# Optimization experiments

Measured on AMD Instinct MI355X. Metric: run time of the kernel, lower is better.

Reference implementation:

```python
import jax, jax.numpy as jnp
import numpy as np

EPS = 1e-5


def setup_inputs() -> dict:
    key = jax.random.key(0)
    ks = jax.random.split(key, 6)
    B, N, F = 8, 8192, 64
    xyzs = jax.random.uniform(ks[0], (B, N, 3), dtype=jnp.float32)
    feats = jax.random.normal(ks[1], (B, N, F), dtype=jnp.float32)
    c_in = 3 + F  # 67
    dims = [(64, c_in), (64, 64), (128, 64)]
    inp = {"xyzs": xyzs, "feats": feats}
    for i, (co, ci) in enumerate(dims, start=1):
        inp[f"w{i}"] = jax.random.normal(ks[1 + i], (co, ci), dtype=jnp.float32) / np.sqrt(ci)
        inp[f"b{i}"] = jnp.zeros((co,), jnp.float32)
        inp[f"g{i}"] = jnp.ones((co,), jnp.float32)
        inp[f"bt{i}"] = jnp.zeros((co,), jnp.float32)
        inp[f"m{i}"] = jnp.zeros((co,), jnp.float32)
        inp[f"v{i}"] = jnp.ones((co,), jnp.float32)
    return inp


def sample_farthest_points(xyz, S):
    # Iterative FPS starting from index 0 (pytorch3d default random_start_point=False).
    B, N, _ = xyz.shape
    barange = jnp.arange(B)

    def step(carry, _):
        mind, last = carry                      # mind: [B,N] min sq-dist to selected set
        lastp = xyz[barange, last]              # [B,3]
        d = jnp.sum((xyz - lastp[:, None, :]) ** 2, -1)
        mind = jnp.minimum(mind, d)
        nxt = jnp.argmax(mind, axis=1).astype(jnp.int32)
        return (mind, nxt), nxt

    init = (jnp.full((B, N), 1e10, xyz.dtype), jnp.zeros((B,), jnp.int32))
    _, rest = jax.lax.scan(step, init, None, length=S - 1)  # [S-1, B]
    idx = jnp.concatenate([jnp.zeros((1, B), jnp.int32), rest], 0).T  # [B,S]
    return xyz[barange[:, None], idx], idx


def ball_query(centers, xyz, K, radius):
    # First-K-in-radius semantics of pytorch3d.ops.ball_query; pad idx with -1,
    # pad gathered points with zeros (masked_gather behavior).
    B, N, _ = xyz.shape
    d2 = (jnp.sum(centers ** 2, -1)[:, :, None]
          + jnp.sum(xyz ** 2, -1)[:, None, :]
          - 2.0 * jnp.einsum('bsd,bnd->bsn', centers, xyz))  # [B,S,N]
    within = d2 <= radius * radius
    skey = jnp.where(within, jnp.arange(N, dtype=jnp.int32), N)
    negvals, idx = jax.lax.top_k(-skey, K)      # K smallest keys = first K in-radius
    valid = (-negvals) < N                       # [B,S,K]
    group_idx = jnp.where(valid, idx, -1)
    gathered = xyz[jnp.arange(B)[:, None, None], jnp.where(valid, idx, 0)]  # [B,S,K,3]
    group_xyz = jnp.where(valid[..., None], gathered, 0.0)
    return group_idx, group_xyz


def _mlp_layer(x, w, b, g, bt, m, v):
    # 1x1 Conv2d over channel axis + BatchNorm (eval stats) + ReLU; x: [B,S,K,Cin]
    y = jnp.einsum('bskc,oc->bsko', x, w) + b
    y = g * (y - m) * jax.lax.rsqrt(v + EPS) + bt
    return jax.nn.relu(y)


def reference(xyzs, feats, w1, b1, g1, bt1, m1, v1,
              w2, b2, g2, bt2, m2, v2, w3, b3, g3, bt3, m3, v3):
    S, K, radius = 2048, 32, 0.2
    B = xyzs.shape[0]
    center_xyzs, _ = sample_farthest_points(xyzs, S)             # [B,S,3]
    group_idxs, group_xyzs = ball_query(center_xyzs, xyzs, K, radius)
    group_xyzs = group_xyzs - center_xyzs[:, :, None, :]          # relative coords
    batch_idxs = jnp.arange(B)[:, None, None]
    gf = feats[batch_idxs, jnp.where(group_idxs < 0, 0, group_idxs)]  # [B,S,K,F]
    gf = jnp.concatenate([group_xyzs, gf], axis=-1)
    gf = gf * (group_idxs != -1)[..., None].astype(gf.dtype)      # zero padded slots
    x = _mlp_layer(gf, w1, b1, g1, bt1, m1, v1)
    x = _mlp_layer(x, w2, b2, g2, bt2, m2, v2)
    x = _mlp_layer(x, w3, b3, g3, bt3, m3, v3)
    center_feats = jnp.max(x, axis=2)                             # max over neighbors
    return center_xyzs, center_feats
```

## Files before the change

### kernel.cpp

```cpp
#include <hip/hip_runtime.h>


#define NPTS 8192
#define SCTR 2048
#define NB   8
#define KNN  32
#define NF   64

typedef float v2f __attribute__((ext_vector_type(2)));

__device__ __forceinline__ v2f pk_add(v2f a, v2f b) {
  v2f r; asm("v_pk_add_f32 %0, %1, %2" : "=v"(r) : "v"(a), "v"(b)); return r;
}
__device__ __forceinline__ v2f pk_mul(v2f a, v2f b) {
  v2f r; asm("v_pk_mul_f32 %0, %1, %2" : "=v"(r) : "v"(a), "v"(b)); return r;
}

__device__ __forceinline__ float sumsq3(float x, float y, float z) {
#pragma clang fp contract(off)
  return (x * x + y * y) + z * z;
}

__device__ __forceinline__ float bq_d2(float sc, float sx,
                                       float cx, float cy, float cz,
                                       float x, float y, float z) {
#pragma clang fp contract(off)
  float dt = fmaf(cz, z, fmaf(cy, y, cx * x));
  return (sc + sx) - 2.0f * dt;
}

template <int CTRL>
__device__ __forceinline__ unsigned long long kmax_dpp(unsigned long long k) {
  int lo = (int)(unsigned int)(k & 0xFFFFFFFFull);
  int hi = (int)(unsigned int)(k >> 32);
  int slo = __builtin_amdgcn_update_dpp(lo, lo, CTRL, 0xF, 0xF, false);
  int shi = __builtin_amdgcn_update_dpp(hi, hi, CTRL, 0xF, 0xF, false);
  unsigned long long sk =
      ((unsigned long long)(unsigned int)shi << 32) | (unsigned int)slo;
  return sk > k ? sk : k;
}

__global__ __launch_bounds__(256, 1) void fps_transpose_kernel(
    const float* __restrict__ xyzs,
    const float* __restrict__ w1, const float* __restrict__ w2, const float* __restrict__ w3,
    float* __restrict__ centers, float* __restrict__ wT)
{
  const int t = threadIdx.x;
  if (blockIdx.x >= NB) {
    int idx = (blockIdx.x - NB) * 256 + t;
    if (idx < 67*64) {
      int c = idx >> 6, o = idx & 63;
      wT[idx] = w1[o*67 + c];
    } else if (idx < 67*64 + 64*64) {
      int r = idx - 67*64; int c = r >> 6, o = r & 63;
      wT[idx] = w2[o*64 + c];
    } else if (idx < 67*64 + 64*64 + 64*128) {
      int r = idx - (67*64 + 64*64); int c = r >> 7, o = r & 127;
      wT[idx] = w3[o*64 + c];
    }
    return;
  }

  const int b = blockIdx.x;
  const float* xb = xyzs + (size_t)b * NPTS * 3;

  __shared__ float sX[NPTS], sY[NPTS], sZ[NPTS];
  __shared__ unsigned long long redk[2][4];
  __shared__ int hist[SCTR];

  for (int i = t; i < NPTS; i += 256) {
    sX[i] = xb[3*i+0];
    sY[i] = xb[3*i+1];
    sZ[i] = xb[3*i+2];
  }
  if (t == 0) hist[0] = 0;
  __syncthreads();

  const int t4 = 4 * t;

  const float4 xA = *(const float4*)(sX + 0    + t4);
  const float4 yA = *(const float4*)(sY + 0    + t4);
  const float4 zA = *(const float4*)(sZ + 0    + t4);
  const float4 xB = *(const float4*)(sX + 1024 + t4);
  const float4 yB = *(const float4*)(sY + 1024 + t4);
  const float4 zB = *(const float4*)(sZ + 1024 + t4);
  const float4 xC = *(const float4*)(sX + 2048 + t4);
  const float4 yC = *(const float4*)(sY + 2048 + t4);
  const float4 zC = *(const float4*)(sZ + 2048 + t4);
  const float4 xD = *(const float4*)(sX + 3072 + t4);
  const float4 yD = *(const float4*)(sY + 3072 + t4);
  const float4 zD = *(const float4*)(sZ + 3072 + t4);
  const float4 xE = *(const float4*)(sX + 4096 + t4);
  const float4 yE = *(const float4*)(sY + 4096 + t4);
  const float4 zE = *(const float4*)(sZ + 4096 + t4);
  const float4 xF = *(const float4*)(sX + 5120 + t4);
  const float4 yF = *(const float4*)(sY + 5120 + t4);
  const float4 zF = *(const float4*)(sZ + 5120 + t4);
  const float4 xG = *(const float4*)(sX + 6144 + t4);
  const float4 yG = *(const float4*)(sY + 6144 + t4);
  const float4 zG = *(const float4*)(sZ + 6144 + t4);
  const float4 xH = *(const float4*)(sX + 7168 + t4);
  const float4 yH = *(const float4*)(sY + 7168 + t4);
  const float4 zH = *(const float4*)(sZ + 7168 + t4);

  float4 mA = make_float4(1e10f,1e10f,1e10f,1e10f);
  float4 mB = mA, mC = mA, mD = mA, mE = mA, mF = mA, mG = mA, mH = mA;

  float lx = sX[0], ly = sY[0], lz = sZ[0];

#define FPS_HALF(PX0, PX1, PY0, PY1, PZ0, PZ1, MM0, MM1, I0, I1, BV, BG)     \
  do {                                                                       \
    v2f px_ = {PX0, PX1}, py_ = {PY0, PY1}, pz_ = {PZ0, PZ1};               \
    v2f dx_ = pk_add(px_, nlx);                                              \
    v2f dy_ = pk_add(py_, nly);                                              \
    v2f dz_ = pk_add(pz_, nlz);                                              \
    v2f dd_ = pk_add(pk_add(pk_mul(dx_,dx_), pk_mul(dy_,dy_)),               \
                     pk_mul(dz_,dz_));                                       \
    MM0 = fminf(MM0, dd_.x); if (MM0 > BV) { BV = MM0; BG = (I0); }          \
    MM1 = fminf(MM1, dd_.y); if (MM1 > BV) { BV = MM1; BG = (I1); }          \
  } while (0)

#define FPS_QUAD(QX, QY, QZ, MV, QOFF, BV, BG)                               \
  do {                                                                       \
    FPS_HALF(QX.x, QX.y, QY.x, QY.y, QZ.x, QZ.y, MV.x, MV.y,                 \
             (QOFF)+t4+0, (QOFF)+t4+1, BV, BG);                              \
    FPS_HALF(QX.z, QX.w, QY.z, QY.w, QZ.z, QZ.w, MV.z, MV.w,                 \
             (QOFF)+t4+2, (QOFF)+t4+3, BV, BG);                              \
  } while (0)

  for (int s = 1; s < SCTR; ++s) {
    float bv0 = -1.0f, bv1 = -1.0f; int bg0 = 0, bg1 = 0;
    {
      v2f nlx = {-lx, -lx}, nly = {-ly, -ly}, nlz = {-lz, -lz};
      FPS_QUAD(xA, yA, zA, mA, 0,    bv0, bg0);
      FPS_QUAD(xB, yB, zB, mB, 1024, bv0, bg0);
      FPS_QUAD(xC, yC, zC, mC, 2048, bv0, bg0);
      FPS_QUAD(xD, yD, zD, mD, 3072, bv0, bg0);
      FPS_QUAD(xE, yE, zE, mE, 4096, bv1, bg1);
      FPS_QUAD(xF, yF, zF, mF, 5120, bv1, bg1);
      FPS_QUAD(xG, yG, zG, mG, 6144, bv1, bg1);
      FPS_QUAD(xH, yH, zH, mH, 7168, bv1, bg1);
    }
    float bv = bv0; int bg = bg0;
    if (bv1 > bv0) { bv = bv1; bg = bg1; }

    unsigned long long key =
        ((unsigned long long)__float_as_uint(bv) << 13) |
        (unsigned long long)(8191 - bg);

    key = kmax_dpp<0x111>(key);
    key = kmax_dpp<0x112>(key);
    key = kmax_dpp<0x114>(key);
    key = kmax_dpp<0x118>(key);
    key = kmax_dpp<0x142>(key);
    key = kmax_dpp<0x143>(key);

    int pb = s & 1;
    if ((t & 63) == 63) redk[pb][t >> 6] = key;
    __syncthreads();

    unsigned long long k4 = redk[pb][t & 3];
    k4 = kmax_dpp<0xB1>(k4);
    k4 = kmax_dpp<0x4E>(k4);

    int i0 = 8191 - (int)(k4 & 0x1FFFull);
    lx = sX[i0]; ly = sY[i0]; lz = sZ[i0];
    if (t == 0) hist[s] = i0;
  }
#undef FPS_QUAD
#undef FPS_HALF
  __syncthreads();

  for (int s = t; s < SCTR; s += 256) {
    int i = hist[s];
    float* o = centers + ((size_t)b * SCTR + s) * 3;
    o[0] = sX[i]; o[1] = sY[i]; o[2] = sZ[i];
  }
}

__global__ __launch_bounds__(128) void sa_fused_kernel(
    const float* __restrict__ xyzs, const float* __restrict__ feats,
    const float* centers, const float* __restrict__ wT,
    const float* __restrict__ b1, const float* __restrict__ g1, const float* __restrict__ bt1,
    const float* __restrict__ m1, const float* __restrict__ v1,
    const float* __restrict__ b2, const float* __restrict__ g2, const float* __restrict__ bt2,
    const float* __restrict__ m2, const float* __restrict__ v2,
    const float* __restrict__ b3, const float* __restrict__ g3, const float* __restrict__ bt3,
    const float* __restrict__ m3, const float* __restrict__ v3,
    float* out_feats)
{
  constexpr float R2 = (float)(0.2 * 0.2);
  const int bid  = blockIdx.x;
  const int b    = bid >> 11;
  const int tid  = threadIdx.x;
  const int w    = tid >> 6;
  const int lane = tid & 63;
  const float* xb = xyzs + (size_t)b * NPTS * 3;
  const float* cp = centers + (size_t)bid * 3;
  float cx = cp[0], cy = cp[1], cz = cp[2];
  float sc = sumsq3(cx, cy, cz);

  __shared__ int   gidx[KNN];
  __shared__ float in_[32*67];
  __shared__ float y_[32*65];

  int cnt = 0;
  for (int base = 0; base < NPTS && cnt < KNN; base += 64) {
    int n = base + lane;
    float x = xb[n*3+0], y = xb[n*3+1], z = xb[n*3+2];
    float sx = sumsq3(x, y, z);
    float d2 = bq_d2(sc, sx, cx, cy, cz, x, y, z);
    bool within = (d2 <= R2);
    unsigned long long mk = __ballot(within);
    int rank = __popcll(mk & ((1ull << lane) - 1ull));
    int slot = cnt + rank;
    if (within && slot < KNN) gidx[slot] = n;
    cnt += (int)__popcll(mk);
  }
  if (cnt > KNN) cnt = KNN;
  __syncthreads();

#pragma unroll 4
  for (int k2 = 0; k2 < 16; ++k2) {
    int k = 2*k2 + w;
    int gk = (k < cnt) ? gidx[k] : -1;
    float fv = 0.f, xv = 0.f;
    if (gk >= 0) {
      fv = feats[((size_t)b * NPTS + gk) * NF + lane];
      if (lane < 3) xv = xb[gk*3 + lane] - cp[lane];
    }
    in_[k*67 + 3 + lane] = fv;
    if (lane < 3) in_[k*67 + lane] = xv;
  }
  __syncthreads();

  const int g = lane >> 3;
  const int h = lane & 7;
  const float* w1T = wT;
  const float* w2T = wT + 67*64;
  const float* w3T = wT + 67*64 + 64*64;

  {
    float acc[4][4];
#pragma unroll
    for (int i=0;i<4;++i)
#pragma unroll
      for (int j=0;j<4;++j) acc[i][j]=0.f;
#pragma unroll 4
    for (int c = 0; c < 67; ++c) {
      float a0 = in_[(4*g+0)*67 + c];
      float a1 = in_[(4*g+1)*67 + c];
      float a2 = in_[(4*g+2)*67 + c];
      float a3 = in_[(4*g+3)*67 + c];
      float4 wv = *(const float4*)(w1T + c*64 + w*32 + 4*h);
      float wj[4] = {wv.x, wv.y, wv.z, wv.w};
#pragma unroll
      for (int j=0;j<4;++j) {
        acc[0][j] = fmaf(a0, wj[j], acc[0][j]);
        acc[1][j] = fmaf(a1, wj[j], acc[1][j]);
        acc[2][j] = fmaf(a2, wj[j], acc[2][j]);
        acc[3][j] = fmaf(a3, wj[j], acc[3][j]);
      }
    }
    float scl[4], shf[4];
#pragma unroll
    for (int j=0;j<4;++j) {
      int o = w*32 + 4*h + j;
      float r = g1[o] * rsqrtf(v1[o] + 1e-5f);
      scl[j] = r;
      shf[j] = (b1[o] - m1[o]) * r + bt1[o];
    }
#pragma unroll
    for (int i=0;i<4;++i) {
      int k = 4*g + i;
#pragma unroll
      for (int j=0;j<4;++j)
        y_[k*65 + w*32 + 4*h + j] = fmaxf(fmaf(acc[i][j], scl[j], shf[j]), 0.f);
    }
  }
  __syncthreads();

  {
    float acc[4][4];
#pragma unroll
    for (int i=0;i<4;++i)
#pragma unroll
      for (int j=0;j<4;++j) acc[i][j]=0.f;
#pragma unroll 4
    for (int c = 0; c < 64; ++c) {
      float a0 = y_[(4*g+0)*65 + c];
      float a1 = y_[(4*g+1)*65 + c];
      float a2 = y_[(4*g+2)*65 + c];
      float a3 = y_[(4*g+3)*65 + c];
      float4 wv = *(const float4*)(w2T + c*64 + w*32 + 4*h);
      float wj[4] = {wv.x, wv.y, wv.z, wv.w};
#pragma unroll
      for (int j=0;j<4;++j) {
        acc[0][j] = fmaf(a0, wj[j], acc[0][j]);
        acc[1][j] = fmaf(a1, wj[j], acc[1][j]);
        acc[2][j] = fmaf(a2, wj[j], acc[2][j]);
        acc[3][j] = fmaf(a3, wj[j], acc[3][j]);
      }
    }
    float scl[4], shf[4];
#pragma unroll
    for (int j=0;j<4;++j) {
      int o = w*32 + 4*h + j;
      float r = g2[o] * rsqrtf(v2[o] + 1e-5f);
      scl[j] = r;
      shf[j] = (b2[o] - m2[o]) * r + bt2[o];
    }
    __syncthreads();
#pragma unroll
    for (int i=0;i<4;++i) {
      int k = 4*g + i;
#pragma unroll
      for (int j=0;j<4;++j)
        in_[k*65 + w*32 + 4*h + j] = fmaxf(fmaf(acc[i][j], scl[j], shf[j]), 0.f);
    }
  }
  __syncthreads();

  for (int p = 0; p < 2; ++p) {
    float acc[4][4];
#pragma unroll
    for (int i=0;i<4;++i)
#pragma unroll
      for (int j=0;j<4;++j) acc[i][j]=0.f;
#pragma unroll 4
    for (int c = 0; c < 64; ++c) {
      float a0 = in_[(4*g+0)*65 + c];
      float a1 = in_[(4*g+1)*65 + c];
      float a2 = in_[(4*g+2)*65 + c];
      float a3 = in_[(4*g+3)*65 + c];
      float4 wv = *(const float4*)(w3T + c*128 + w*64 + p*32 + 4*h);
      float wj[4] = {wv.x, wv.y, wv.z, wv.w};
#pragma unroll
      for (int j=0;j<4;++j) {
        acc[0][j] = fmaf(a0, wj[j], acc[0][j]);
        acc[1][j] = fmaf(a1, wj[j], acc[1][j]);
        acc[2][j] = fmaf(a2, wj[j], acc[2][j]);
        acc[3][j] = fmaf(a3, wj[j], acc[3][j]);
      }
    }
    float scl[4], shf[4];
#pragma unroll
    for (int j=0;j<4;++j) {
      int o = w*64 + p*32 + 4*h + j;
      float r = g3[o] * rsqrtf(v3[o] + 1e-5f);
      scl[j] = r;
      shf[j] = (b3[o] - m3[o]) * r + bt3[o];
    }
    float vm[4];
#pragma unroll
    for (int j=0;j<4;++j) {
      float q0 = fmaxf(fmaf(acc[0][j], scl[j], shf[j]), 0.f);
      float q1 = fmaxf(fmaf(acc[1][j], scl[j], shf[j]), 0.f);
      float q2 = fmaxf(fmaf(acc[2][j], scl[j], shf[j]), 0.f);
      float q3 = fmaxf(fmaf(acc[3][j], scl[j], shf[j]), 0.f);
      vm[j] = fmaxf(fmaxf(q0,q1), fmaxf(q2,q3));
    }
#pragma unroll
    for (int mk = 8; mk < 64; mk <<= 1) {
#pragma unroll
      for (int j=0;j<4;++j) vm[j] = fmaxf(vm[j], __shfl_xor(vm[j], mk));
    }
    if (g == 0) {
      float* dst = out_feats + (size_t)bid*128 + w*64 + p*32 + 4*h;
      *(float4*)dst = make_float4(vm[0], vm[1], vm[2], vm[3]);
    }
  }
}

extern "C" void kernel_launch(void* const* d_in, const int* in_sizes, int n_in,
                              void* d_out, int out_size, void* d_ws, size_t ws_size,
                              hipStream_t stream) {
  const float* xyzs  = (const float*)d_in[0];
  const float* feats = (const float*)d_in[1];
  const float* w1  = (const float*)d_in[2];
  const float* b1  = (const float*)d_in[3];
  const float* g1  = (const float*)d_in[4];
  const float* bt1 = (const float*)d_in[5];
  const float* m1  = (const float*)d_in[6];
  const float* v1  = (const float*)d_in[7];
  const float* w2  = (const float*)d_in[8];
  const float* b2  = (const float*)d_in[9];
  const float* g2  = (const float*)d_in[10];
  const float* bt2 = (const float*)d_in[11];
  const float* m2  = (const float*)d_in[12];
  const float* v2  = (const float*)d_in[13];
  const float* w3  = (const float*)d_in[14];
  const float* b3  = (const float*)d_in[15];
  const float* g3  = (const float*)d_in[16];
  const float* bt3 = (const float*)d_in[17];
  const float* m3  = (const float*)d_in[18];
  const float* v3  = (const float*)d_in[19];

  float* out       = (float*)d_out;
  float* centers   = out;
  float* out_feats = out + (size_t)NB * SCTR * 3;
  float* wT        = (float*)d_ws;

  hipLaunchKernelGGL(fps_transpose_kernel, dim3(NB + 65), dim3(256), 0, stream,
                     xyzs, w1, w2, w3, centers, wT);
  hipLaunchKernelGGL(sa_fused_kernel, dim3(NB * SCTR), dim3(128), 0, stream,
                     xyzs, feats, centers, wT,
                     b1, g1, bt1, m1, v1,
                     b2, g2, bt2, m2, v2,
                     b3, g3, bt3, m3, v3,
                     out_feats);
}
```

Before: 2.389 ms.

## Pad MLP activation rows to 68 for float4 LDS access; scalarize FPS distance

Shared-memory activation buffers are padded from 67/65 to 68-float rows. The MLP inner loops now read four channels at once with float4 LDS loads, take four weight rows per step, and write outputs as float4, which cuts the number of LDS instructions. The first layer zero-fills column 67 and loops to 68, so it reads one row past the end of w1T (the start of w2T); that read is harmless because it is multiplied by zero. The FPS loop also drops the inline-asm packed v_pk_add/v_pk_mul math in favour of plain scalar distance code with contraction off, which may change instruction count in the serial FPS phase.

```diff
diff --git a/kernel.cpp b/kernel.cpp
--- a/kernel.cpp
+++ b/kernel.cpp
@@ -7,18 +7,18 @@
 #define KNN  32
 #define NF   64
 
-typedef float v2f __attribute__((ext_vector_type(2)));
-
-__device__ __forceinline__ v2f pk_add(v2f a, v2f b) {
-  v2f r; asm("v_pk_add_f32 %0, %1, %2" : "=v"(r) : "v"(a), "v"(b)); return r;
-}
-__device__ __forceinline__ v2f pk_mul(v2f a, v2f b) {
-  v2f r; asm("v_pk_mul_f32 %0, %1, %2" : "=v"(r) : "v"(a), "v"(b)); return r;
-}
-
 __device__ __forceinline__ float sumsq3(float x, float y, float z) {
 #pragma clang fp contract(off)
   return (x * x + y * y) + z * z;
+}
+
+__device__ __forceinline__ float fps_sqdist(float ax, float ay, float az,
+                                            float bx, float by, float bz) {
+#pragma clang fp contract(off)
+  float dx = ax - bx;
+  float dy = ay - by;
+  float dz = az - bz;
+  return (dx * dx + dy * dy) + dz * dz;
 }
 
 __device__ __forceinline__ float bq_d2(float sc, float sx,
@@ -108,39 +108,30 @@
 
   float lx = sX[0], ly = sY[0], lz = sZ[0];
 
-#define FPS_HALF(PX0, PX1, PY0, PY1, PZ0, PZ1, MM0, MM1, I0, I1, BV, BG)     \
-  do {                                                                       \
-    v2f px_ = {PX0, PX1}, py_ = {PY0, PY1}, pz_ = {PZ0, PZ1};               \
-    v2f dx_ = pk_add(px_, nlx);                                              \
-    v2f dy_ = pk_add(py_, nly);                                              \
-    v2f dz_ = pk_add(pz_, nlz);                                              \
-    v2f dd_ = pk_add(pk_add(pk_mul(dx_,dx_), pk_mul(dy_,dy_)),               \
-                     pk_mul(dz_,dz_));                                       \
-    MM0 = fminf(MM0, dd_.x); if (MM0 > BV) { BV = MM0; BG = (I0); }          \
-    MM1 = fminf(MM1, dd_.y); if (MM1 > BV) { BV = MM1; BG = (I1); }          \
-  } while (0)
-
-#define FPS_QUAD(QX, QY, QZ, MV, QOFF, BV, BG)                               \
-  do {                                                                       \
-    FPS_HALF(QX.x, QX.y, QY.x, QY.y, QZ.x, QZ.y, MV.x, MV.y,                 \
-             (QOFF)+t4+0, (QOFF)+t4+1, BV, BG);                              \
-    FPS_HALF(QX.z, QX.w, QY.z, QY.w, QZ.z, QZ.w, MV.z, MV.w,                 \
-             (QOFF)+t4+2, (QOFF)+t4+3, BV, BG);                              \
+#define FPS_QUAD(QX, QY, QZ, MV, QOFF, BV, BG)                                  \
+  do {                                                                          \
+    float d;                                                                    \
+    d = fps_sqdist(QX.x, QY.x, QZ.x, lx, ly, lz);                               \
+    MV.x = fminf(MV.x, d); if (MV.x > BV) { BV = MV.x; BG = (QOFF)+t4+0; }      \
+    d = fps_sqdist(QX.y, QY.y, QZ.y, lx, ly, lz);                               \
+    MV.y = fminf(MV.y, d); if (MV.y > BV) { BV = MV.y; BG = (QOFF)+t4+1; }      \
+    d = fps_sqdist(QX.z, QY.z, QZ.z, lx, ly, lz);                               \
+    MV.z = fminf(MV.z, d); if (MV.z > BV) { BV = MV.z; BG = (QOFF)+t4+2; }      \
+    d = fps_sqdist(QX.w, QY.w, QZ.w, lx, ly, lz);                               \
+    MV.w = fminf(MV.w, d); if (MV.w > BV) { BV = MV.w; BG = (QOFF)+t4+3; }      \
   } while (0)
 
   for (int s = 1; s < SCTR; ++s) {
     float bv0 = -1.0f, bv1 = -1.0f; int bg0 = 0, bg1 = 0;
-    {
-      v2f nlx = {-lx, -lx}, nly = {-ly, -ly}, nlz = {-lz, -lz};
-      FPS_QUAD(xA, yA, zA, mA, 0,    bv0, bg0);
-      FPS_QUAD(xB, yB, zB, mB, 1024, bv0, bg0);
-      FPS_QUAD(xC, yC, zC, mC, 2048, bv0, bg0);
-      FPS_QUAD(xD, yD, zD, mD, 3072, bv0, bg0);
-      FPS_QUAD(xE, yE, zE, mE, 4096, bv1, bg1);
-      FPS_QUAD(xF, yF, zF, mF, 5120, bv1, bg1);
-      FPS_QUAD(xG, yG, zG, mG, 6144, bv1, bg1);
-      FPS_QUAD(xH, yH, zH, mH, 7168, bv1, bg1);
-    }
+    FPS_QUAD(xA, yA, zA, mA, 0,    bv0, bg0);
+    FPS_QUAD(xB, yB, zB, mB, 1024, bv0, bg0);
+    FPS_QUAD(xC, yC, zC, mC, 2048, bv0, bg0);
+    FPS_QUAD(xD, yD, zD, mD, 3072, bv0, bg0);
+    FPS_QUAD(xE, yE, zE, mE, 4096, bv1, bg1);
+    FPS_QUAD(xF, yF, zF, mF, 5120, bv1, bg1);
+    FPS_QUAD(xG, yG, zG, mG, 6144, bv1, bg1);
+    FPS_QUAD(xH, yH, zH, mH, 7168, bv1, bg1);
+
     float bv = bv0; int bg = bg0;
     if (bv1 > bv0) { bv = bv1; bg = bg1; }
 
@@ -168,7 +159,6 @@
     if (t == 0) hist[s] = i0;
   }
 #undef FPS_QUAD
-#undef FPS_HALF
   __syncthreads();
 
   for (int s = t; s < SCTR; s += 256) {
@@ -201,8 +191,8 @@
   float sc = sumsq3(cx, cy, cz);
 
   __shared__ int   gidx[KNN];
-  __shared__ float in_[32*67];
-  __shared__ float y_[32*65];
+  __shared__ float in_[32*68];
+  __shared__ float y_[32*68];
 
   int cnt = 0;
   for (int base = 0; base < NPTS && cnt < KNN; base += 64) {
@@ -229,53 +219,73 @@
       fv = feats[((size_t)b * NPTS + gk) * NF + lane];
       if (lane < 3) xv = xb[gk*3 + lane] - cp[lane];
     }
-    in_[k*67 + 3 + lane] = fv;
-    if (lane < 3) in_[k*67 + lane] = xv;
-  }
-  __syncthreads();
-
-  const int g = lane >> 3;
-  const int h = lane & 7;
+    in_[k*68 + 3 + lane] = fv;
+    if (lane < 3) in_[k*68 + lane] = xv;
+    if (lane == 3) in_[k*68 + 67] = 0.f;
+  }
+  __syncthreads();
+
+  const int g  = lane >> 3;
+  const int h  = lane & 7;
+  const int ob = w*32 + 4*h;
   const float* w1T = wT;
   const float* w2T = wT + 67*64;
   const float* w3T = wT + 67*64 + 64*64;
 
+#define FMA_COL(AS0, AS1, AS2, AS3, WV)                                      \
+  do {                                                                       \
+    acc[0][0]=fmaf(AS0, WV.x, acc[0][0]); acc[0][1]=fmaf(AS0, WV.y, acc[0][1]); \
+    acc[0][2]=fmaf(AS0, WV.z, acc[0][2]); acc[0][3]=fmaf(AS0, WV.w, acc[0][3]); \
+    acc[1][0]=fmaf(AS1, WV.x, acc[1][0]); acc[1][1]=fmaf(AS1, WV.y, acc[1][1]); \
+    acc[1][2]=fmaf(AS1, WV.z, acc[1][2]); acc[1][3]=fmaf(AS1, WV.w, acc[1][3]); \
+    acc[2][0]=fmaf(AS2, WV.x, acc[2][0]); acc[2][1]=fmaf(AS2, WV.y, acc[2][1]); \
+    acc[2][2]=fmaf(AS2, WV.z, acc[2][2]); acc[2][3]=fmaf(AS2, WV.w, acc[2][3]); \
+    acc[3][0]=fmaf(AS3, WV.x, acc[3][0]); acc[3][1]=fmaf(AS3, WV.y, acc[3][1]); \
+    acc[3][2]=fmaf(AS3, WV.z, acc[3][2]); acc[3][3]=fmaf(AS3, WV.w, acc[3][3]); \
+  } while (0)
+
+#define MLP_CHUNK(SRC, WBASE, WSTRIDE, WOFF)                                 \
+  do {                                                                       \
+    float4 a0 = *(const float4*)(SRC + (4*g+0)*68 + c0);                     \
+    float4 a1 = *(const float4*)(SRC + (4*g+1)*68 + c0);                     \
+    float4 a2 = *(const float4*)(SRC + (4*g+2)*68 + c0);                     \
+    float4 a3 = *(const float4*)(SRC + (4*g+3)*68 + c0);                     \
+    float4 wv0 = *(const float4*)(WBASE + (c0+0)*(WSTRIDE) + (WOFF));        \
+    float4 wv1 = *(const float4*)(WBASE + (c0+1)*(WSTRIDE) + (WOFF));        \
+    float4 wv2 = *(const float4*)(WBASE + (c0+2)*(WSTRIDE) + (WOFF));        \
+    float4 wv3 = *(const float4*)(WBASE + (c0+3)*(WSTRIDE) + (WOFF));        \
+    FMA_COL(a0.x, a1.x, a2.x, a3.x, wv0);                                    \
+    FMA_COL(a0.y, a1.y, a2.y, a3.y, wv1);                                    \
+    FMA_COL(a0.z, a1.z, a2.z, a3.z, wv2);                                    \
+    FMA_COL(a0.w, a1.w, a2.w, a3.w, wv3);                                    \
+  } while (0)
+
   {
     float acc[4][4];
 #pragma unroll
     for (int i=0;i<4;++i)
 #pragma unroll
       for (int j=0;j<4;++j) acc[i][j]=0.f;
-#pragma unroll 4
-    for (int c = 0; c < 67; ++c) {
-      float a0 = in_[(4*g+0)*67 + c];
-      float a1 = in_[(4*g+1)*67 + c];
-      float a2 = in_[(4*g+2)*67 + c];
-      float a3 = in_[(4*g+3)*67 + c];
-      float4 wv = *(const float4*)(w1T + c*64 + w*32 + 4*h);
-      float wj[4] = {wv.x, wv.y, wv.z, wv.w};
-#pragma unroll
-      for (int j=0;j<4;++j) {
-        acc[0][j] = fmaf(a0, wj[j], acc[0][j]);
-        acc[1][j] = fmaf(a1, wj[j], acc[1][j]);
-        acc[2][j] = fmaf(a2, wj[j], acc[2][j]);
-        acc[3][j] = fmaf(a3, wj[j], acc[3][j]);
-      }
+#pragma unroll 2
+    for (int c0 = 0; c0 < 68; c0 += 4) {
+      MLP_CHUNK(in_, w1T, 64, ob);
     }
     float scl[4], shf[4];
 #pragma unroll
     for (int j=0;j<4;++j) {
-      int o = w*32 + 4*h + j;
+      int o = ob + j;
       float r = g1[o] * rsqrtf(v1[o] + 1e-5f);
       scl[j] = r;
       shf[j] = (b1[o] - m1[o]) * r + bt1[o];
     }
 #pragma unroll
     for (int i=0;i<4;++i) {
-      int k = 4*g + i;
-#pragma unroll
-      for (int j=0;j<4;++j)
-        y_[k*65 + w*32 + 4*h + j] = fmaxf(fmaf(acc[i][j], scl[j], shf[j]), 0.f);
+      float4 out;
+      out.x = fmaxf(fmaf(acc[i][0], scl[0], shf[0]), 0.f);
+      out.y = fmaxf(fmaf(acc[i][1], scl[1], shf[1]), 0.f);
+      out.z = fmaxf(fmaf(acc[i][2], scl[2], shf[2]), 0.f);
+      out.w = fmaxf(fmaf(acc[i][3], scl[3], shf[3]), 0.f);
+      *(float4*)(y_ + (4*g+i)*68 + ob) = out;
     }
   }
   __syncthreads();
@@ -286,26 +296,14 @@
     for (int i=0;i<4;++i)
 #pragma unroll
       for (int j=0;j<4;++j) acc[i][j]=0.f;
-#pragma unroll 4
-    for (int c = 0; c < 64; ++c) {
-      float a0 = y_[(4*g+0)*65 + c];
-      float a1 = y_[(4*g+1)*65 + c];
-      float a2 = y_[(4*g+2)*65 + c];
-      float a3 = y_[(4*g+3)*65 + c];
-      float4 wv = *(const float4*)(w2T + c*64 + w*32 + 4*h);
-      float wj[4] = {wv.x, wv.y, wv.z, wv.w};
-#pragma unroll
-      for (int j=0;j<4;++j) {
-        acc[0][j] = fmaf(a0, wj[j], acc[0][j]);
-        acc[1][j] = fmaf(a1, wj[j], acc[1][j]);
-        acc[2][j] = fmaf(a2, wj[j], acc[2][j]);
-        acc[3][j] = fmaf(a3, wj[j], acc[3][j]);
-      }
+#pragma unroll 2
+    for (int c0 = 0; c0 < 64; c0 += 4) {
+      MLP_CHUNK(y_, w2T, 64, ob);
     }
     float scl[4], shf[4];
 #pragma unroll
     for (int j=0;j<4;++j) {
-      int o = w*32 + 4*h + j;
+      int o = ob + j;
       float r = g2[o] * rsqrtf(v2[o] + 1e-5f);
       scl[j] = r;
       shf[j] = (b2[o] - m2[o]) * r + bt2[o];
@@ -313,40 +311,31 @@
     __syncthreads();
 #pragma unroll
     for (int i=0;i<4;++i) {
-      int k = 4*g + i;
-#pragma unroll
-      for (int j=0;j<4;++j)
-        in_[k*65 + w*32 + 4*h + j] = fmaxf(fmaf(acc[i][j], scl[j], shf[j]), 0.f);
+      float4 out;
+      out.x = fmaxf(fmaf(acc[i][0], scl[0], shf[0]), 0.f);
+      out.y = fmaxf(fmaf(acc[i][1], scl[1], shf[1]), 0.f);
+      out.z = fmaxf(fmaf(acc[i][2], scl[2], shf[2]), 0.f);
+      out.w = fmaxf(fmaf(acc[i][3], scl[3], shf[3]), 0.f);
+      *(float4*)(in_ + (4*g+i)*68 + ob) = out;
     }
   }
   __syncthreads();
 
   for (int p = 0; p < 2; ++p) {
+    const int o3 = w*64 + p*32 + 4*h;
     float acc[4][4];
 #pragma unroll
     for (int i=0;i<4;++i)
 #pragma unroll
       for (int j=0;j<4;++j) acc[i][j]=0.f;
-#pragma unroll 4
-    for (int c = 0; c < 64; ++c) {
-      float a0 = in_[(4*g+0)*65 + c];
-      float a1 = in_[(4*g+1)*65 + c];
-      float a2 = in_[(4*g+2)*65 + c];
-      float a3 = in_[(4*g+3)*65 + c];
-      float4 wv = *(const float4*)(w3T + c*128 + w*64 + p*32 + 4*h);
-      float wj[4] = {wv.x, wv.y, wv.z, wv.w};
-#pragma unroll
-      for (int j=0;j<4;++j) {
-        acc[0][j] = fmaf(a0, wj[j], acc[0][j]);
-        acc[1][j] = fmaf(a1, wj[j], acc[1][j]);
-        acc[2][j] = fmaf(a2, wj[j], acc[2][j]);
-        acc[3][j] = fmaf(a3, wj[j], acc[3][j]);
-      }
+#pragma unroll 2
+    for (int c0 = 0; c0 < 64; c0 += 4) {
+      MLP_CHUNK(in_, w3T, 128, o3);
     }
     float scl[4], shf[4];
 #pragma unroll
     for (int j=0;j<4;++j) {
-      int o = w*64 + p*32 + 4*h + j;
+      int o = o3 + j;
       float r = g3[o] * rsqrtf(v3[o] + 1e-5f);
       scl[j] = r;
       shf[j] = (b3[o] - m3[o]) * r + bt3[o];
@@ -366,10 +355,12 @@
       for (int j=0;j<4;++j) vm[j] = fmaxf(vm[j], __shfl_xor(vm[j], mk));
     }
     if (g == 0) {
-      float* dst = out_feats + (size_t)bid*128 + w*64 + p*32 + 4*h;
+      float* dst = out_feats + (size_t)bid*128 + o3;
       *(float4*)dst = make_float4(vm[0], vm[1], vm[2], vm[3]);
     }
   }
+#undef MLP_CHUNK
+#undef FMA_COL
 }
 
 extern "C" void kernel_launch(void* const* d_in, const int* in_sizes, int n_in,
```

Measured after the change: 2.468 ms. +3.3%, slower.
